# Performance work log

Hardware: AMD Instinct MI355X
Metric: run time of the kernel (lower is better)

Reference implementation:

```python
import jax, jax.numpy as jnp
import numpy as np

N_HEADS, D_MODEL, D_HEAD = 16, 1024, 64
INIT_STD = 0.02
IGNORE = -100000.0


def setup_inputs() -> dict:
    key = jax.random.key(0)
    ks = jax.random.split(key, 5)
    x = jax.random.normal(ks[0], (2, 2048, D_MODEL), dtype=jnp.float32)
    W_Q = INIT_STD * jax.random.normal(ks[1], (N_HEADS, D_MODEL, D_HEAD), dtype=jnp.float32)
    W_K = INIT_STD * jax.random.normal(ks[2], (N_HEADS, D_MODEL, D_HEAD), dtype=jnp.float32)
    W_V = INIT_STD * jax.random.normal(ks[3], (N_HEADS, D_MODEL, D_HEAD), dtype=jnp.float32)
    W_O = INIT_STD * jax.random.normal(ks[4], (N_HEADS, D_HEAD, D_MODEL), dtype=jnp.float32)
    b_Q = jnp.zeros((N_HEADS, D_HEAD), dtype=jnp.float32)
    b_K = jnp.zeros((N_HEADS, D_HEAD), dtype=jnp.float32)
    b_V = jnp.zeros((N_HEADS, D_HEAD), dtype=jnp.float32)
    b_O = jnp.zeros((D_MODEL,), dtype=jnp.float32)
    return {"normalized_resid_pre": x, "W_Q": W_Q, "W_K": W_K, "W_V": W_V,
            "W_O": W_O, "b_Q": b_Q, "b_K": b_K, "b_V": b_V, "b_O": b_O}


def reference(normalized_resid_pre, W_Q, W_K, W_V, W_O, b_Q, b_K, b_V, b_O):
    x = normalized_resid_pre  # [b, s, d_model]
    q = jnp.einsum('bsm,hmd->bshd', x, W_Q) + b_Q  # [b, s, h, d_head]
    k = jnp.einsum('bsm,hmd->bshd', x, W_K) + b_K
    v = jnp.einsum('bsm,hmd->bshd', x, W_V) + b_V
    scores = jnp.einsum('bqhd,bkhd->bhqk', q, k) / jnp.sqrt(jnp.float32(D_HEAD))
    s = x.shape[1]
    causal = jnp.triu(jnp.ones((s, s), dtype=bool), k=1)  # True above diagonal
    scores = jnp.where(causal, jnp.float32(IGNORE), scores)
    pattern = jax.nn.softmax(scores, axis=-1)  # [b, h, q, k]
    z = jnp.einsum('bkhd,bhqk->bqhd', v, pattern)
    attn_out = jnp.einsum('bqhd,hdm->bqm', z, W_O) + b_O
    return attn_out
```

## Files before the change

### kernel.cpp

```cpp
#include <hip/hip_runtime.h>
#include <hip/hip_bf16.h>

#define BB   2
#define SS   2048
#define HH   16
#define DM_  1024
#define DH_  64
#define NROW 4096
#define NQKV 3072

typedef unsigned short u16;
typedef unsigned int u32;
using short4v = __attribute__((ext_vector_type(4))) short;
using short8 = __attribute__((ext_vector_type(8))) short;
using bf16x8 = __attribute__((ext_vector_type(8))) __bf16;
using f32x4  = __attribute__((ext_vector_type(4))) float;
using f32x16 = __attribute__((ext_vector_type(16))) float;

#define QSCALE 0.180336880f

__device__ __forceinline__ u16 f2bf(float f) {
    union { float f; unsigned u; } v; v.f = f;
    unsigned r = v.u + 0x7fffu + ((v.u >> 16) & 1u);
    return (u16)(r >> 16);
}

__device__ __forceinline__ f32x4 mfma16(bf16x8 a, bf16x8 b, f32x4 c) {
    return __builtin_amdgcn_mfma_f32_16x16x32_bf16(a, b, c, 0, 0, 0);
}
__device__ __forceinline__ f32x16 mfma32(bf16x8 a, bf16x8 b, f32x16 c) {
    return __builtin_amdgcn_mfma_f32_32x32x16_bf16(a, b, c, 0, 0, 0);
}

__device__ __forceinline__ u32 cvtpk(float lo, float hi) {
    u32 r;
    asm("v_cvt_pk_bf16_f32 %0, %1, %2" : "=v"(r) : "v"(lo), "v"(hi));
    return r;
}
#define PLSWAP(a, b) asm("v_permlane32_swap_b32 %0, %1" : "+v"(a), "+v"(b))

__device__ __forceinline__ float fexp2(float x) {
#if __has_builtin(__builtin_amdgcn_exp2f)
    return __builtin_amdgcn_exp2f(x);
#else
    float r; asm("v_exp_f32 %0, %1" : "=v"(r) : "v"(x)); return r;
#endif
}

__device__ __forceinline__ void gload16(const void* g, void* l) {
    __builtin_amdgcn_global_load_lds(
        (const __attribute__((address_space(1))) void*)g,
        (__attribute__((address_space(3))) void*)l, 16, 0, 0);
}

__global__ __launch_bounds__(256)
void prep(const float* __restrict__ x,  const float* __restrict__ wq,
          const float* __restrict__ wk, const float* __restrict__ wv,
          const float* __restrict__ wo, const float* __restrict__ bq,
          const float* __restrict__ bk, const float* __restrict__ bv,
          u16* __restrict__ Xb, u16* __restrict__ Wt,
          u16* __restrict__ WoT, float* __restrict__ biasQKV) {
    __shared__ float tile[64][65];
    const int bx = blockIdx.x, t = threadIdx.x;
    if (bx < 512) {
        const int tid = bx * 256 + t;
        #pragma unroll
        for (int it = 0; it < 8; ++it) {
            int i = tid + it * 131072;
            float4 v = ((const float4*)x)[i];
            u16 b4[4] = {f2bf(v.x), f2bf(v.y), f2bf(v.z), f2bf(v.w)};
            ((short4v*)Xb)[i] = *(short4v*)b4;
        }
        if (tid < NQKV) {
            int mat = tid >> 10, h = (tid >> 6) & 15, d = tid & 63;
            const float* bb = (mat == 0) ? bq : ((mat == 1) ? bk : bv);
            biasQKV[tid] = bb[h * DH_ + d];
        }
    } else if (bx < 1280) {
        const int idx = bx - 512;
        const int m0 = (idx & 15) * 64, hm = idx >> 4;
        const int mat = hm >> 4, h = hm & 15;
        const float* w = (mat == 0) ? wq : ((mat == 1) ? wk : wv);
        #pragma unroll
        for (int it = 0; it < 4; ++it) {
            int row = it * 16 + (t >> 4), c4 = (t & 15) * 4;
            float4 v = *(const float4*)&w[((size_t)h * 1024 + m0 + row) * 64 + c4];
            tile[row][c4] = v.x; tile[row][c4 + 1] = v.y;
            tile[row][c4 + 2] = v.z; tile[row][c4 + 3] = v.w;
        }
        __syncthreads();
        #pragma unroll
        for (int it = 0; it < 2; ++it) {
            int c = it * 256 + t, d = c >> 3, mc = (c & 7) * 8;
            u16 buf[8];
            #pragma unroll
            for (int j = 0; j < 8; ++j) buf[j] = f2bf(tile[mc + j][d]);
            *(short8*)&Wt[((size_t)(mat * 1024 + h * 64 + d)) * 1024 + m0 + mc] = *(short8*)buf;
        }
    } else {
        const int idx = bx - 1280;
        const int n0 = (idx & 15) * 64, k0 = (idx >> 4) * 64;
        #pragma unroll
        for (int it = 0; it < 4; ++it) {
            int row = it * 16 + (t >> 4), c4 = (t & 15) * 4;
            float4 v = *(const float4*)&wo[(size_t)(k0 + row) * DM_ + n0 + c4];
            tile[row][c4] = v.x; tile[row][c4 + 1] = v.y;
            tile[row][c4 + 2] = v.z; tile[row][c4 + 3] = v.w;
        }
        __syncthreads();
        #pragma unroll
        for (int it = 0; it < 2; ++it) {
            int c = it * 256 + t, n = c >> 3, kc = (c & 7) * 8;
            u16 buf[8];
            #pragma unroll
            for (int j = 0; j < 8; ++j) buf[j] = f2bf(tile[kc + j][n]);
            *(short8*)&WoT[(size_t)(n0 + n) * DM_ + k0 + kc] = *(short8*)buf;
        }
    }
}

__device__ __forceinline__ void gemm_core_128(
    const u16* __restrict__ Ap, const u16* __restrict__ Bp,
    int brow, int bcol, u16* lds, f32x4 acc[4][2]) {
    const int t = threadIdx.x, l = t & 63;
    const int wid = t >> 6, wm = wid >> 2, wn = wid & 3;
    const int c0 = t, c1 = t + 512;
    const int r0 = c0 >> 3, sb0 = ((c0 & 7) ^ (r0 & 7)) << 3;
    const int r1 = c1 >> 3, sb1 = ((c1 & 7) ^ (r1 & 7)) << 3;
    u16* A0 = lds;
    u16* B0 = lds + 16384;
    const int rA0 = wm * 64 + (l & 15);
    const int rB0 = wn * 32 + (l & 15);
    const int sw  = (l & 7) << 3;
    const int colA = ((l >> 4) << 3);

    {
        gload16(Ap + (size_t)(brow + r0) * DM_ + sb0, A0 + c0 * 8);
        gload16(Ap + (size_t)(brow + r1) * DM_ + sb1, A0 + c1 * 8);
        gload16(Bp + (size_t)(bcol + r0) * DM_ + sb0, B0 + c0 * 8);
        gload16(Bp + (size_t)(bcol + r1) * DM_ + sb1, B0 + c1 * 8);
    }
    __syncthreads();
    for (int kt = 0; kt < 16; ++kt) {
        const int p = kt & 1;
        if (kt < 15) {
            const int ko = (kt + 1) * 64;
            gload16(Ap + (size_t)(brow + r0) * DM_ + ko + sb0, A0 + (p ^ 1) * 8192 + c0 * 8);
            gload16(Ap + (size_t)(brow + r1) * DM_ + ko + sb1, A0 + (p ^ 1) * 8192 + c1 * 8);
            gload16(Bp + (size_t)(bcol + r0) * DM_ + ko + sb0, B0 + (p ^ 1) * 8192 + c0 * 8);
            gload16(Bp + (size_t)(bcol + r1) * DM_ + ko + sb1, B0 + (p ^ 1) * 8192 + c1 * 8);
        }
        const u16* Ab = A0 + p * 8192;
        const u16* Bb = B0 + p * 8192;
        #pragma unroll
        for (int kc = 0; kc < 64; kc += 32) {
            const int cx = (kc + colA) ^ sw;
            bf16x8 af[4], bfr[2];
            #pragma unroll
            for (int m = 0; m < 4; ++m)
                af[m] = *(const bf16x8*)(Ab + (rA0 + m * 16) * 64 + cx);
            #pragma unroll
            for (int n = 0; n < 2; ++n)
                bfr[n] = *(const bf16x8*)(Bb + (rB0 + n * 16) * 64 + cx);
            __builtin_amdgcn_s_setprio(1);
            #pragma unroll
            for (int m = 0; m < 4; ++m)
                #pragma unroll
                for (int n = 0; n < 2; ++n)
                    acc[m][n] = mfma16(af[m], bfr[n], acc[m][n]);
            __builtin_amdgcn_s_setprio(0);
        }
        __syncthreads();
    }
}

__global__ __launch_bounds__(512)
void gemm_qkv3(const u16* __restrict__ Xb, const u16* __restrict__ Wt,
               const float* __restrict__ bias, u16* __restrict__ Qs,
               u16* __restrict__ Ks, u16* __restrict__ Vt) {
    __shared__ __align__(16) u16 lds[32768];
    const int bx = blockIdx.x, t = threadIdx.x, l = t & 63;
    const int wid = t >> 6, wm = wid >> 2, wn = wid & 3;
    f32x4 acc[4][2] = {};
    const bool isV = (bx >= 512);
    int brow, bcol; const u16 *Ap, *Bp;
    if (!isV) { brow = (bx & 31) * 128; bcol = (bx >> 5) * 128; Ap = Xb; Bp = Wt; }
    else { int i2 = bx - 512; brow = (i2 & 7) * 128; bcol = (i2 >> 3) * 128;
           Ap = Wt + (size_t)2048 * DM_; Bp = Xb; }
    gemm_core_128(Ap, Bp, brow, bcol, lds, acc);

    u16* wr_ = lds + wid * 2048;
    const int colbase = bcol + wn * 32;
    const int rowbase = brow + wm * 64;
    const int rsub = ((l >> 4) << 2);
    if (!isV) {
        const float b0 = bias[colbase + (l & 15)];
        const float b1 = bias[colbase + 16 + (l & 15)];
        const float scl = (colbase < 1024) ? QSCALE : 1.0f;
        #pragma unroll
        for (int m = 0; m < 4; ++m)
            #pragma unroll
            for (int n = 0; n < 2; ++n) {
                const float bb = n ? b1 : b0;
                #pragma unroll
                for (int r = 0; r < 4; ++r)
                    wr_[(m * 16 + rsub + r) * 32 + n * 16 + (l & 15)] =
                        f2bf((acc[m][n][r] + bb) * scl);
            }
    } else {
        #pragma unroll
        for (int m = 0; m < 4; ++m) {
            float4 bv = *(const float4*)&bias[2048 + rowbase + m * 16 + rsub];
            const float bbr[4] = {bv.x, bv.y, bv.z, bv.w};
            #pragma unroll
            for (int n = 0; n < 2; ++n)
                #pragma unroll
                for (int r = 0; r < 4; ++r)
                    wr_[(m * 16 + rsub + r) * 32 + n * 16 + (l & 15)] =
                        f2bf(acc[m][n][r] + bbr[r]);
        }
    }
    __syncthreads();
    if (!isV) {
        const int hsel = (colbase >> 6) & 15, d0 = colbase & 63;
        const int bsel = rowbase >> 11, s0 = rowbase & 2047;
        u16* outp = (colbase < 1024) ? Qs : Ks;
        #pragma unroll
        for (int p = 0; p < 4; ++p) {
            const int rr = p * 16 + (l >> 2);
            short8 v = *(const short8*)(wr_ + rr * 32 + (l & 3) * 8);
            *(short8*)&outp[(((size_t)bsel * HH + hsel) * SS + s0 + rr) * DH_ + d0 + (l & 3) * 8] = v;
        }
    } else {
        const int bsel = colbase >> 11, s0 = colbase & 2047;
        #pragma unroll
        for (int p = 0; p < 4; ++p) {
            const int rr = p * 16 + (l >> 2);
            short8 v = *(const short8*)(wr_ + rr * 32 + (l & 3) * 8);
            *(short8*)&Vt[((size_t)bsel * 1024 + rowbase + rr) * SS + s0 + (l & 3) * 8] = v;
        }
    }
}

__global__ __launch_bounds__(512)
void gemm_out3(const u16* __restrict__ Zb, const u16* __restrict__ WoT,
               const float* __restrict__ bO, float* __restrict__ out) {
    __shared__ __align__(16) u16 lds[32768];
    const int bx = blockIdx.x, t = threadIdx.x, l = t & 63;
    const int wid = t >> 6, wm = wid >> 2, wn = wid & 3;
    const int brow = (bx & 31) * 128, bcol = (bx >> 5) * 128;
    f32x4 acc[4][2] = {};
    gemm_core_128(Zb, WoT, brow, bcol, lds, acc);
    const int colbase = bcol + wn * 32;
    const int rowbase = brow + wm * 64;
    const int rsub = ((l >> 4) << 2);
    const float b0 = bO[colbase + (l & 15)];
    const float b1 = bO[colbase + 16 + (l & 15)];
    #pragma unroll
    for (int m = 0; m < 4; ++m)
        #pragma unroll
        for (int n = 0; n < 2; ++n) {
            const float bb = n ? b1 : b0;
            #pragma unroll
            for (int r = 0; r < 4; ++r)
                out[(size_t)(rowbase + m * 16 + rsub + r) * DM_ + colbase + n * 16 + (l & 15)] =
                    acc[m][n][r] + bb;
        }
}

__global__ __launch_bounds__(512, 4)
void attn_fwd(const u16* __restrict__ Qs, const u16* __restrict__ Ks,
              const u16* __restrict__ Vt, u16* __restrict__ Zb) {
    __shared__ __align__(16) u16 fK[2][8192];
    __shared__ __align__(16) u16 fV[2][8192];
    __shared__ float lrP[128];
    __shared__ float lrX[128];
    const int bidx = blockIdx.x;
    const int j  = (bidx < 256) ? (15 - (bidx >> 5)) : ((bidx - 256) >> 5);
    const int bh = bidx & 31, b = bh >> 4, h = bh & 15;
    const int t = threadIdx.x, wid = t >> 6, l = t & 63;
    const int hi = l >> 5, c32 = l & 31;
    const int qh = wid >> 1, par = wid & 1;
    const u16* Qp = Qs + (size_t)bh * SS * DH_;
    const u16* Kp = Ks + (size_t)bh * SS * DH_;
    const u16* Vp = Vt + (size_t)bh * DH_ * SS;
    const int qw = j * 128 + qh * 32;
    const int nr = j + 1;

    bf16x8 aq[4];
    #pragma unroll
    for (int dk = 0; dk < 4; ++dk)
        aq[dk] = *(const bf16x8*)&Qp[(size_t)(qw + c32) * DH_ + dk * 16 + hi * 8];

    int kOff[2]; size_t vOff[2]; int dstc[2];
    #pragma unroll
    for (int i = 0; i < 2; ++i) {
        const int c = t + 512 * i, sec = c >> 6, ln = c & 63;
        const int kh = sec >> 3, s7 = sec & 7;
        kOff[i] = (kh * 64 + (s7 >> 2) * 32 + (ln & 31)) * DH_ + (s7 & 3) * 16 + (ln >> 5) * 8;
        vOff[i] = (size_t)((s7 >> 2) * 32 + (ln & 31)) * SS + kh * 64 + (s7 & 3) * 16 + (ln >> 5) * 8;
        dstc[i] = c * 8;
    }

    #define ISSUE(rr, pb)                                                     \
    {   const int ka = (rr) * 128;                                            \
        gload16(Kp + (size_t)ka * DH_ + kOff[0], &fK[pb][dstc[0]]);           \
        gload16(Kp + (size_t)ka * DH_ + kOff[1], &fK[pb][dstc[1]]);           \
        gload16(Vp + ka + vOff[0], &fV[pb][dstc[0]]);                         \
        gload16(Vp + ka + vOff[1], &fV[pb][dstc[1]]);                         \
    }

    ISSUE(0, 0)
    __syncthreads();

    f32x16 o0 = {}, o1 = {};
    float lrp[4] = {0.f, 0.f, 0.f, 0.f};

    for (int r = 0; r < nr; ++r) {
        const int p = r & 1;
        if (r + 1 < nr) ISSUE(r + 1, p ^ 1)
        const int kv0 = r * 128 + par * 64;
        if (kv0 <= qw + 31) {
            const u16* fKb = &fK[p][par * 4096];
            const u16* fVb = &fV[p][par * 4096];
            const bool have1 = (kv0 + 32 <= qw + 31);
            f32x16 s0 = {}, s1 = {};
            __builtin_amdgcn_s_setprio(1);
            #pragma unroll
            for (int dk = 0; dk < 4; ++dk)
                s0 = mfma32(*(const bf16x8*)(fKb + dk * 512 + l * 8), aq[dk], s0);
            if (have1) {
                #pragma unroll
                for (int dk = 0; dk < 4; ++dk)
                    s1 = mfma32(*(const bf16x8*)(fKb + (4 + dk) * 512 + l * 8), aq[dk], s1);
            }
            __builtin_amdgcn_s_setprio(0);
            if (kv0 + 63 > qw) {
                const int q = qw + c32;
                #pragma unroll
                for (int r16 = 0; r16 < 16; ++r16) {
                    const int crow = (r16 & 3) + 8 * (r16 >> 2) + 4 * hi;
                    if (kv0 + crow > q) s0[r16] = -1e30f;
                }
                if (have1) {
                    #pragma unroll
                    for (int r16 = 0; r16 < 16; ++r16) {
                        const int crow = (r16 & 3) + 8 * (r16 >> 2) + 4 * hi;
                        if (kv0 + 32 + crow > q) s1[r16] = -1e30f;
                    }
                }
            }
            #pragma unroll
            for (int r16 = 0; r16 < 16; ++r16) {
                s0[r16] = fexp2(s0[r16]);
                lrp[r16 & 3] += s0[r16];
            }
            if (have1) {
                #pragma unroll
                for (int r16 = 0; r16 < 16; ++r16) {
                    s1[r16] = fexp2(s1[r16]);
                    lrp[r16 & 3] += s1[r16];
                }
            }
            __builtin_amdgcn_s_setprio(1);
            #define PV_STEP(PS, B8, KS)                                          \
            {                                                                    \
                u32 cA  = cvtpk(PS[B8 + 0], PS[B8 + 1]);                         \
                u32 cA2 = cvtpk(PS[B8 + 2], PS[B8 + 3]);                         \
                u32 cB  = cvtpk(PS[B8 + 4], PS[B8 + 5]);                         \
                u32 cB2 = cvtpk(PS[B8 + 6], PS[B8 + 7]);                         \
                PLSWAP(cA, cB); PLSWAP(cA2, cB2);                                \
                u32 w[4] = {cA, cA2, cB, cB2};                                   \
                bf16x8 pa = *(bf16x8*)w;                                         \
                o0 = mfma32(pa, *(const bf16x8*)(fVb + (0 * 4 + (KS)) * 512 + l * 8), o0); \
                o1 = mfma32(pa, *(const bf16x8*)(fVb + (1 * 4 + (KS)) * 512 + l * 8), o1); \
            }
            PV_STEP(s0, 0, 0)
            PV_STEP(s0, 8, 1)
            if (have1) {
                PV_STEP(s1, 0, 2)
                PV_STEP(s1, 8, 3)
            }
            #undef PV_STEP
            __builtin_amdgcn_s_setprio(0);
        }
        __syncthreads();
    }
    #undef ISSUE

    float lrow = (lrp[0] + lrp[1]) + (lrp[2] + lrp[3]);
    lrow += __shfl_xor(lrow, 32);

    float* mrg = (float*)fK;
    __syncthreads();
    if (par) {
        #pragma unroll
        for (int e = 0; e < 16; ++e) mrg[qh * 2048 + e * 64 + l] = o0[e];
        #pragma unroll
        for (int e = 0; e < 16; ++e) mrg[qh * 2048 + (16 + e) * 64 + l] = o1[e];
        if (hi == 0) lrP[qh * 32 + c32] = lrow;
    }
    __syncthreads();
    if (!par) {
        #pragma unroll
        for (int e = 0; e < 16; ++e) o0[e] += mrg[qh * 2048 + e * 64 + l];
        #pragma unroll
        for (int e = 0; e < 16; ++e) o1[e] += mrg[qh * 2048 + (16 + e) * 64 + l];
        lrow += lrP[qh * 32 + c32];
        lrX[qh * 32 + c32] = lrow;
        float invv[16];
        #pragma unroll
        for (int g = 0; g < 4; ++g) {
            float4 lv = *(const float4*)&lrX[qh * 32 + 8 * g + 4 * hi];
            invv[g * 4 + 0] = 1.0f / lv.x;
            invv[g * 4 + 1] = 1.0f / lv.y;
            invv[g * 4 + 2] = 1.0f / lv.z;
            invv[g * 4 + 3] = 1.0f / lv.w;
        }
        #pragma unroll
        for (int r16 = 0; r16 < 16; ++r16) {
            const int q = qw + (r16 & 3) + 8 * (r16 >> 2) + 4 * hi;
            u16* zp = &Zb[(((size_t)b * SS + q) * HH + h) * DH_];
            zp[c32]      = f2bf(o0[r16] * invv[r16]);
            zp[32 + c32] = f2bf(o1[r16] * invv[r16]);
        }
    }
}

extern "C" void kernel_launch(void* const* d_in, const int* in_sizes, int n_in,
                              void* d_out, int out_size, void* d_ws, size_t ws_size,
                              hipStream_t stream) {
    const float* x  = (const float*)d_in[0];
    const float* wq = (const float*)d_in[1];
    const float* wk = (const float*)d_in[2];
    const float* wv = (const float*)d_in[3];
    const float* wo = (const float*)d_in[4];
    const float* bq = (const float*)d_in[5];
    const float* bk = (const float*)d_in[6];
    const float* bv = (const float*)d_in[7];
    const float* bO = (const float*)d_in[8];
    float* out = (float*)d_out;

    char* w = (char*)d_ws;
    u16* Xb  = (u16*)w;  w += (size_t)NROW * DM_ * 2;
    u16* Wt  = (u16*)w;  w += (size_t)NQKV * DM_ * 2;
    u16* WoT = (u16*)w;  w += (size_t)DM_ * DM_ * 2;
    float* biasQKV = (float*)w; w += (size_t)NQKV * 4;
    u16* Qs  = (u16*)w;  w += (size_t)BB * HH * SS * DH_ * 2;
    u16* Ks  = (u16*)w;  w += (size_t)BB * HH * SS * DH_ * 2;
    u16* Vt  = (u16*)w;  w += (size_t)BB * HH * SS * DH_ * 2;
    u16* Zb  = (u16*)w;  w += (size_t)BB * HH * SS * DH_ * 2;

    prep<<<1536, 256, 0, stream>>>(x, wq, wk, wv, wo, bq, bk, bv,
                                   Xb, Wt, WoT, biasQKV);
    gemm_qkv3<<<768, 512, 0, stream>>>(Xb, Wt, biasQKV, Qs, Ks, Vt);
    attn_fwd<<<512, 512, 0, stream>>>(Qs, Ks, Vt, Zb);
    gemm_out3<<<256, 512, 0, stream>>>(Zb, WoT, bO, out);
}
```

Measured before the change: 95.52 us.

## Split long causal attention q-tiles across two blocks with a merge kernel

Query tiles 7-15 are split into two blocks that each process alternating KV tiles, writing unnormalized fp32 partial outputs and row sums to workspace. A new merge kernel adds the halves and normalizes them into Zb. A static schedule table orders the work so the longest pieces start first. This is meant to balance load and fill more CUs during causal attention, at the cost of an extra launch and extra global traffic for the partials. The merge relies on a fixed softmax max (no running max), so adding partials directly is valid.

```diff
diff --git a/kernel.cpp b/kernel.cpp
--- a/kernel.cpp
+++ b/kernel.cpp
@@ -52,6 +52,9 @@
         (const __attribute__((address_space(1))) void*)g,
         (__attribute__((address_space(3))) void*)l, 16, 0, 0);
 }
+
+__device__ const int SCHED_QT[25]   = {15,15,14,14,13,13,12,6,12,11,11,10,5,10,9,9,8,4,8,7,7,3,2,1,0};
+__device__ const int SCHED_HALF[25] = { 0, 1, 0, 1, 0, 1, 0,2, 1, 0, 1, 0,2, 1,0,1,0,2,1,0,1,2,2,2,2};
 
 __global__ __launch_bounds__(256)
 void prep(const float* __restrict__ x,  const float* __restrict__ wq,
@@ -270,22 +273,28 @@
 
 __global__ __launch_bounds__(512, 4)
 void attn_fwd(const u16* __restrict__ Qs, const u16* __restrict__ Ks,
-              const u16* __restrict__ Vt, u16* __restrict__ Zb) {
+              const u16* __restrict__ Vt, u16* __restrict__ Zb,
+              float* __restrict__ Po, float* __restrict__ Pl) {
     __shared__ __align__(16) u16 fK[2][8192];
     __shared__ __align__(16) u16 fV[2][8192];
     __shared__ float lrP[128];
     __shared__ float lrX[128];
     const int bidx = blockIdx.x;
-    const int j  = (bidx < 256) ? (15 - (bidx >> 5)) : ((bidx - 256) >> 5);
+    const int e  = bidx >> 5;
     const int bh = bidx & 31, b = bh >> 4, h = bh & 15;
+    const int qt = SCHED_QT[e], half = SCHED_HALF[e];
+    const bool issplit = (half < 2);
+    const int nr = qt + 1;
+    const int step = issplit ? 2 : 1;
+    const int rfirst = issplit ? half : 0;
+    const int cnt = issplit ? ((nr - half + 1) >> 1) : nr;
     const int t = threadIdx.x, wid = t >> 6, l = t & 63;
     const int hi = l >> 5, c32 = l & 31;
     const int qh = wid >> 1, par = wid & 1;
     const u16* Qp = Qs + (size_t)bh * SS * DH_;
     const u16* Kp = Ks + (size_t)bh * SS * DH_;
     const u16* Vp = Vt + (size_t)bh * DH_ * SS;
-    const int qw = j * 128 + qh * 32;
-    const int nr = j + 1;
+    const int qw = qt * 128 + qh * 32;
 
     bf16x8 aq[4];
     #pragma unroll
@@ -310,15 +319,16 @@
         gload16(Vp + ka + vOff[1], &fV[pb][dstc[1]]);                         \
     }
 
-    ISSUE(0, 0)
+    ISSUE(rfirst, 0)
     __syncthreads();
 
     f32x16 o0 = {}, o1 = {};
     float lrp[4] = {0.f, 0.f, 0.f, 0.f};
 
-    for (int r = 0; r < nr; ++r) {
-        const int p = r & 1;
-        if (r + 1 < nr) ISSUE(r + 1, p ^ 1)
+    int r = rfirst;
+    for (int i = 0; i < cnt; ++i, r += step) {
+        const int p = i & 1;
+        if (i + 1 < cnt) ISSUE(r + step, p ^ 1)
         const int kv0 = r * 128 + par * 64;
         if (kv0 <= qw + 31) {
             const u16* fKb = &fK[p][par * 4096];
@@ -395,36 +405,71 @@
     __syncthreads();
     if (par) {
         #pragma unroll
-        for (int e = 0; e < 16; ++e) mrg[qh * 2048 + e * 64 + l] = o0[e];
-        #pragma unroll
-        for (int e = 0; e < 16; ++e) mrg[qh * 2048 + (16 + e) * 64 + l] = o1[e];
+        for (int e2 = 0; e2 < 16; ++e2) mrg[qh * 2048 + e2 * 64 + l] = o0[e2];
+        #pragma unroll
+        for (int e2 = 0; e2 < 16; ++e2) mrg[qh * 2048 + (16 + e2) * 64 + l] = o1[e2];
         if (hi == 0) lrP[qh * 32 + c32] = lrow;
     }
     __syncthreads();
     if (!par) {
         #pragma unroll
-        for (int e = 0; e < 16; ++e) o0[e] += mrg[qh * 2048 + e * 64 + l];
-        #pragma unroll
-        for (int e = 0; e < 16; ++e) o1[e] += mrg[qh * 2048 + (16 + e) * 64 + l];
+        for (int e2 = 0; e2 < 16; ++e2) o0[e2] += mrg[qh * 2048 + e2 * 64 + l];
+        #pragma unroll
+        for (int e2 = 0; e2 < 16; ++e2) o1[e2] += mrg[qh * 2048 + (16 + e2) * 64 + l];
         lrow += lrP[qh * 32 + c32];
-        lrX[qh * 32 + c32] = lrow;
-        float invv[16];
-        #pragma unroll
-        for (int g = 0; g < 4; ++g) {
-            float4 lv = *(const float4*)&lrX[qh * 32 + 8 * g + 4 * hi];
-            invv[g * 4 + 0] = 1.0f / lv.x;
-            invv[g * 4 + 1] = 1.0f / lv.y;
-            invv[g * 4 + 2] = 1.0f / lv.z;
-            invv[g * 4 + 3] = 1.0f / lv.w;
-        }
-        #pragma unroll
-        for (int r16 = 0; r16 < 16; ++r16) {
-            const int q = qw + (r16 & 3) + 8 * (r16 >> 2) + 4 * hi;
-            u16* zp = &Zb[(((size_t)b * SS + q) * HH + h) * DH_];
-            zp[c32]      = f2bf(o0[r16] * invv[r16]);
-            zp[32 + c32] = f2bf(o1[r16] * invv[r16]);
-        }
-    }
+        if (issplit) {
+            float* po = Po + ((size_t)((bh * 9 + (qt - 7)) * 2 + half)) * 8192;
+            #pragma unroll
+            for (int r16 = 0; r16 < 16; ++r16) {
+                const int lq = qh * 32 + (r16 & 3) + 8 * (r16 >> 2) + 4 * hi;
+                po[lq * 64 + c32]      = o0[r16];
+                po[lq * 64 + 32 + c32] = o1[r16];
+            }
+            if (hi == 0)
+                Pl[((bh * 9 + (qt - 7)) * 2 + half) * 128 + qh * 32 + c32] = lrow;
+        } else {
+            lrX[qh * 32 + c32] = lrow;
+            float invv[16];
+            #pragma unroll
+            for (int g = 0; g < 4; ++g) {
+                float4 lv = *(const float4*)&lrX[qh * 32 + 8 * g + 4 * hi];
+                invv[g * 4 + 0] = 1.0f / lv.x;
+                invv[g * 4 + 1] = 1.0f / lv.y;
+                invv[g * 4 + 2] = 1.0f / lv.z;
+                invv[g * 4 + 3] = 1.0f / lv.w;
+            }
+            #pragma unroll
+            for (int r16 = 0; r16 < 16; ++r16) {
+                const int q = qw + (r16 & 3) + 8 * (r16 >> 2) + 4 * hi;
+                u16* zp = &Zb[(((size_t)b * SS + q) * HH + h) * DH_];
+                zp[c32]      = f2bf(o0[r16] * invv[r16]);
+                zp[32 + c32] = f2bf(o1[r16] * invv[r16]);
+            }
+        }
+    }
+}
+
+__global__ __launch_bounds__(256)
+void attn_merge(const float* __restrict__ Po, const float* __restrict__ Pl,
+                u16* __restrict__ Zb) {
+    const int gid = blockIdx.x * 256 + threadIdx.x;
+    if (gid >= 32 * 9 * 128 * 16) return;
+    const int row = gid >> 4, dc = (gid & 15) * 4;
+    const int bhq = row >> 7, lq = row & 127;
+    const int bh = bhq / 9, qti = bhq - bh * 9;
+    const int qt = qti + 7;
+    const size_t baseA = ((size_t)(bh * 9 + qti) * 2) * 8192 + (size_t)lq * 64 + dc;
+    const float* A = Po + baseA;
+    const float* B = A + 8192;
+    const float lA = Pl[((bh * 9 + qti) * 2) * 128 + lq];
+    const float lB = Pl[((bh * 9 + qti) * 2 + 1) * 128 + lq];
+    const float inv = 1.0f / (lA + lB);
+    const int b = bh >> 4, h = bh & 15;
+    const int q = qt * 128 + lq;
+    u16 o4[4];
+    #pragma unroll
+    for (int i = 0; i < 4; ++i) o4[i] = f2bf((A[i] + B[i]) * inv);
+    *(short4v*)&Zb[(((size_t)b * SS + q) * HH + h) * DH_ + dc] = *(short4v*)o4;
 }
 
 extern "C" void kernel_launch(void* const* d_in, const int* in_sizes, int n_in,
@@ -450,10 +495,13 @@
     u16* Ks  = (u16*)w;  w += (size_t)BB * HH * SS * DH_ * 2;
     u16* Vt  = (u16*)w;  w += (size_t)BB * HH * SS * DH_ * 2;
     u16* Zb  = (u16*)w;  w += (size_t)BB * HH * SS * DH_ * 2;
+    float* Po = (float*)w; w += (size_t)32 * 9 * 2 * 128 * 64 * 4;
+    float* Pl = (float*)w; w += (size_t)32 * 9 * 2 * 128 * 4;
 
     prep<<<1536, 256, 0, stream>>>(x, wq, wk, wv, wo, bq, bk, bv,
                                    Xb, Wt, WoT, biasQKV);
     gemm_qkv3<<<768, 512, 0, stream>>>(Xb, Wt, biasQKV, Qs, Ks, Vt);
-    attn_fwd<<<512, 512, 0, stream>>>(Qs, Ks, Vt, Zb);
+    attn_fwd<<<800, 512, 0, stream>>>(Qs, Ks, Vt, Zb, Po, Pl);
+    attn_merge<<<2304, 256, 0, stream>>>(Po, Pl, Zb);
     gemm_out3<<<256, 512, 0, stream>>>(Zb, WoT, bO, out);
 }
```

Measured after the change: 96.48 us. Within noise of the previous version (+1.0%).
